# Kernel tuning notes

Hardware: AMD Instinct MI355X
Metric: run time of the kernel (lower is better)

Reference implementation:

```python
import jax, jax.numpy as jnp
import numpy as np

P = 3  # patchsize
EMB = 1024  # pretrain/target embed dimension


def adaptive_avg_pool1d(x, T):
    """torch.F.adaptive_avg_pool1d over last axis (static boundaries)."""
    L = x.shape[-1]
    i = np.arange(T)
    starts = (i * L) // T
    ends = -((-(i + 1) * L) // T)  # ceil((i+1)*L/T)
    cs = jnp.cumsum(x, axis=-1)
    cs = jnp.concatenate([jnp.zeros(x.shape[:-1] + (1,), x.dtype), cs], axis=-1)
    return (cs[..., ends] - cs[..., starts]) / jnp.asarray(ends - starts, x.dtype)


def patchify(x):
    """nn.Unfold(kernel=3, stride=1, pad=1): [B,C,H,W] -> [B,H*W,C,3,3]."""
    B, C, H, W = x.shape
    xp = jnp.pad(x, ((0, 0), (0, 0), (1, 1), (1, 1)))
    pats = jnp.stack([xp[:, :, i:i + H, j:j + W] for i in range(P) for j in range(P)], axis=2)
    pats = pats.reshape(B, C, P, P, H * W).transpose(0, 4, 1, 2, 3)
    return pats, (H, W)


def embed(feat2, feat3):
    B = feat2.shape[0]
    f2, (h0, w0) = patchify(feat2)   # [B, h0*w0, 512, 3, 3]
    f3, (h1, w1) = patchify(feat3)   # [B, h1*w1, 1024, 3, 3]
    C3 = feat3.shape[1]
    # align layer3 patch grid to layer2 grid (bilinear, align_corners=False)
    f3 = f3.reshape(B, h1, w1, C3, P, P).transpose(0, 3, 4, 5, 1, 2)
    f3 = f3.reshape(-1, h1, w1)
    f3 = jax.image.resize(f3, (f3.shape[0], h0, w0), method='bilinear')
    f3 = f3.reshape(B, C3, P, P, h0, w0).transpose(0, 4, 5, 1, 2, 3)
    f3 = f3.reshape(B, h0 * w0, C3, P, P)
    # Preprocessing: MeanMapper per layer -> [N, 2, 1024]
    feats = []
    for f in (f2, f3):
        flat = f.reshape(-1, 1, f.shape[-3] * P * P)       # [N, 1, C*9]
        feats.append(adaptive_avg_pool1d(flat, EMB)[:, 0, :])
    x = jnp.stack(feats, axis=1)                           # [N, 2, 1024]
    # Aggregator: adaptive pool over flattened [N, 1, 2048] -> [N, 1024]
    x = adaptive_avg_pool1d(x.reshape(x.shape[0], 1, -1), EMB)[:, 0, :]
    return x, (h0, w0)


def setup_inputs() -> dict:
    key = jax.random.key(0)
    k1, k2, k3 = jax.random.split(key, 3)
    feat2 = jax.random.normal(k1, (8, 512, 28, 28), dtype=jnp.float32)
    feat3 = jax.random.normal(k2, (8, 1024, 14, 14), dtype=jnp.float32)
    memory_bank = jax.random.normal(k3, (16384, 1024), dtype=jnp.float32)
    return {"feat2": feat2, "feat3": feat3, "memory_bank": memory_bank}


def reference(feat2, feat3, memory_bank):
    B = feat2.shape[0]
    q, (h0, w0) = embed(feat2, feat3)                      # [B*h0*w0, 1024]
    # squared-L2 1-NN against the memory bank (faiss IndexFlatL2, k=1)
    d2 = (jnp.sum(q * q, axis=-1, keepdims=True)
          - 2.0 * (q @ memory_bank.T)
          + jnp.sum(memory_bank * memory_bank, axis=-1)[None, :])
    patch_scores = jnp.min(d2, axis=-1).reshape(B, h0, w0)  # unpatch_scores
    image_scores = jnp.max(patch_scores.reshape(B, -1), axis=-1)  # PatchMaker.score
    return image_scores, patch_scores
```

## Files before the change

### kernel.cpp

```cpp
#include <hip/hip_runtime.h>
#include <hip/hip_bf16.h>

typedef signed char i8;
typedef unsigned char u8;
typedef unsigned short u16;
typedef unsigned int u32;
typedef __attribute__((ext_vector_type(4))) int i32x4;

#define GLD16(g, l) __builtin_amdgcn_global_load_lds((const __attribute__((address_space(1))) u32*)(g), (__attribute__((address_space(3))) u32*)(l), 16, 0, 0)

#define SB (4.5f / 127.f)
#define SQ (2.0f / 127.f)
#define INV_SB (127.f / 4.5f)
#define INV_SQ (127.f / 2.0f)
#define TWO_S (2.0f * SB * SQ)

__device__ __forceinline__ u32 flipf(float f) {
    u32 u = __float_as_uint(f);
    return (u >> 31) ? ~u : (u | 0x80000000u);
}

__device__ __forceinline__ float unflipf(u32 k) {
    return __uint_as_float((k >> 31) ? (k ^ 0x80000000u) : ~k);
}

__device__ __forceinline__ int q8(float x, float invs) {
    return __float2int_rn(fminf(fmaxf(x * invs, -127.f), 127.f));
}

__device__ __forceinline__ void taps(int o, int& i0, int& i1, float& w0, float& w1) {
    int k = (o - 1) >> 1;
    float fy = (0.5f * (float)o - 0.25f) - (float)k;
    i0 = k; i1 = k + 1;
    w0 = 1.0f - fy; w1 = fy;
    if (i0 < 0)  { i0 = 0;  w0 = 0.0f; w1 = 1.0f; }
    if (i1 > 13) { i1 = 13; w1 = 0.0f; w0 = 1.0f; }
}

__global__ __launch_bounds__(256) void prep_kernel(
    const float* __restrict__ f3, float* __restrict__ U,
    const float* __restrict__ mb, u8* __restrict__ mbb, float* __restrict__ mb2,
    u32* __restrict__ minkey, float* __restrict__ qn2) {
    int bid = blockIdx.x, tid = threadIdx.x;
    if (bid < 16384) {
        float4 v = ((const float4*)(mb + (size_t)bid * 1024))[tid];
        u32 p = ((u32)(u8)(i8)q8(v.x, INV_SB))
              | ((u32)(u8)(i8)q8(v.y, INV_SB) << 8)
              | ((u32)(u8)(i8)q8(v.z, INV_SB) << 16)
              | ((u32)(u8)(i8)q8(v.w, INV_SB) << 24);
        ((u32*)(mbb + (size_t)bid * 1024))[tid] = p;
        float ssq = v.x * v.x + v.y * v.y + v.z * v.z + v.w * v.w;
        for (int s = 32; s; s >>= 1) ssq += __shfl_down(ssq, s);
        __shared__ float sm[4];
        if ((tid & 63) == 0) sm[tid >> 6] = ssq;
        __syncthreads();
        if (tid == 0) mb2[bid] = sm[0] + sm[1] + sm[2] + sm[3];
        if (bid < 25) {
            int i = bid * 256 + tid;
            if (i < 6400) minkey[i] = 0xFFFFFFFFu;
        } else if (bid < 50) {
            int i = (bid - 25) * 256 + tid;
            if (i < 6272) qn2[i] = 0.f;
        }
    } else {
        int idx = (bid - 16384) * 256 + tid;
        if (idx >= 8 * 512 * 196) return;
        int b = idx / (512 * 196);
        int rem = idx % (512 * 196);
        int t = rem / 196;
        int yx = rem % 196;
        int y = yx / 14, x = yx % 14;
        const float* p0 = f3 + ((size_t)(b * 1024 + 2 * t)) * 196;
        const float* p1 = p0 + 196;
        float s = 0.f;
        #pragma unroll
        for (int dy = -1; dy <= 1; ++dy) {
            int yy = y + dy; if ((unsigned)yy >= 14u) continue;
            #pragma unroll
            for (int dx = -1; dx <= 1; ++dx) {
                int xx = x + dx; if ((unsigned)xx >= 14u) continue;
                s += p0[yy * 14 + xx] + p1[yy * 14 + xx];
            }
        }
        U[idx] = s;
    }
}

__global__ __launch_bounds__(256) void q_kernel(const float* __restrict__ feat2, const float* __restrict__ U,
                                                u8* __restrict__ qb, float* __restrict__ qn2) {
    __shared__ float lds[3 * 64 * 29];
    const int bid = blockIdx.x;
    const int tid = threadIdx.x;
    const int b = bid / (28 * 16);
    const int rem = bid % (28 * 16);
    const int h = rem / 16;
    const int chunk = rem % 16;
    const int lane = tid & 63;
    const int wg = tid >> 6;

    if (chunk < 8) {
        const int c0 = chunk * 64;
        for (int i = tid; i < 3 * 64 * 28; i += 256) {
            int r = i / 1792;
            int rr = i % 1792;
            int c = rr / 28, x = rr % 28;
            int y = h - 1 + r;
            lds[(r * 64 + c) * 29 + x] = ((unsigned)y < 28u)
                ? feat2[((size_t)(b * 512 + c0 + c) * 28 + y) * 28 + x] : 0.f;
        }
        __syncthreads();
        const float* rowp = &lds[lane * 29];
        #pragma unroll
        for (int wi = 0; wi < 7; ++wi) {
            const int w = wg * 7 + wi;
            float s = 0.f;
            #pragma unroll
            for (int r = 0; r < 3; ++r) {
                #pragma unroll
                for (int dx = -1; dx <= 1; ++dx) {
                    int x = w + dx;
                    if ((unsigned)x >= 28u) continue;
                    float wt = (r == 1 && dx == 0) ? 2.f : 1.f;
                    s += wt * rowp[r * 64 * 29 + x];
                }
            }
            float val = s * 0.1f;
            const int n = b * 784 + h * 28 + w;
            qb[(size_t)n * 1024 + c0 + lane] = (u8)(i8)q8(val, INV_SQ);
            float ss = val * val;
            for (int sft = 32; sft; sft >>= 1) ss += __shfl_down(ss, sft);
            if (lane == 0) atomicAdd(&qn2[n], ss);
        }
    } else {
        const int t0 = (chunk - 8) * 64;
        int y0, y1; float wy0, wy1;
        taps(h, y0, y1, wy0, wy1);
        for (int i = tid; i < 2 * 64 * 14; i += 256) {
            int r = i / 896;
            int rr = i % 896;
            int t = rr / 14, x = rr % 14;
            lds[(r * 64 + t) * 15 + x] =
                U[(size_t)(b * 512 + t0 + t) * 196 + (r ? y1 : y0) * 14 + x];
        }
        __syncthreads();
        const float* rp0 = &lds[lane * 15];
        const float* rp1 = &lds[(64 + lane) * 15];
        #pragma unroll
        for (int wi = 0; wi < 7; ++wi) {
            const int w = wg * 7 + wi;
            int x0, x1; float wx0, wx1;
            taps(w, x0, x1, wx0, wx1);
            float val = (wy0 * (wx0 * rp0[x0] + wx1 * rp0[x1])
                       + wy1 * (wx0 * rp1[x0] + wx1 * rp1[x1])) * (1.f / 18.f);
            const int n = b * 784 + h * 28 + w;
            qb[(size_t)n * 1024 + 512 + t0 + lane] = (u8)(i8)q8(val, INV_SQ);
            float ss = val * val;
            for (int sft = 32; sft; sft >>= 1) ss += __shfl_down(ss, sft);
            if (lane == 0) atomicAdd(&qn2[n], ss);
        }
    }
}

__global__ __launch_bounds__(512, 4) void gemm_min_kernel(
    const u8* __restrict__ qb, const u8* __restrict__ mbb,
    const float* __restrict__ qn2, const float* __restrict__ mb2,
    u32* __restrict__ minkeys) {
    __shared__ __align__(16) u8 As[2][8192];
    __shared__ __align__(16) u8 Bs[2][16384];
    __shared__ u32 rowmin[128];

    const int tid = threadIdx.x;
    const int wid = tid >> 6;
    const int lane = tid & 63;
    const int wm = wid >> 2;
    const int wn = wid & 3;

    const int flat = blockIdx.x;
    const int swz = (flat & 7) * 400 + (flat >> 3);
    const int q0 = (swz % 50) * 128;
    const int m0 = (swz / 50) * 256;

    const int rloc = wid * 16 + (lane >> 2);
    const int sslot = (lane & 3) ^ ((lane >> 3) & 3);
    const size_t gA  = (size_t)(q0 + rloc) * 1024 + sslot * 16;
    const size_t gB0 = (size_t)(m0 + rloc) * 1024 + sslot * 16;
    const size_t gB1 = (size_t)(m0 + 128 + rloc) * 1024 + sslot * 16;
    const u32 ldA = wid * 1024;
    const u32 ldB1 = 8192 + wid * 1024;

    #define STAGE(T) { const int _t = (T); \
        GLD16(qb + gA + _t * 64, &As[_t & 1][ldA]); \
        GLD16(mbb + gB0 + _t * 64, &Bs[_t & 1][ldA]); \
        GLD16(mbb + gB1 + _t * 64, &Bs[_t & 1][ldB1]); }

    const u32 arow = (u32)(wm * 64 + (lane & 15)) * 64;
    const u32 brow = (u32)(wn * 64 + (lane & 15)) * 64;
    const u32 sl = (u32)(((lane >> 4) ^ (((lane & 15) >> 1) & 3)) * 16);

    i32x4 acc[4][4] = {};
    i32x4 a[4], b[4];

    STAGE(0);
    asm volatile("s_waitcnt vmcnt(0)" ::: "memory");
    __builtin_amdgcn_s_barrier();
    __builtin_amdgcn_sched_barrier(0);

    for (int t = 0; t < 16; ++t) {
        const u8* Ab = &As[t & 1][0];
        const u8* Bb = &Bs[t & 1][0];

        #pragma unroll
        for (int m = 0; m < 4; ++m) a[m] = *(const i32x4*)&Ab[arow + m * 1024 + sl];
        #pragma unroll
        for (int n = 0; n < 4; ++n) b[n] = *(const i32x4*)&Bb[brow + n * 1024 + sl];

        if (t < 15) STAGE(t + 1)

        asm volatile("s_waitcnt lgkmcnt(2)" ::: "memory");
        __builtin_amdgcn_sched_barrier(0);
        __builtin_amdgcn_s_setprio(1);
        #pragma unroll
        for (int m = 0; m < 4; ++m)
            #pragma unroll
            for (int n = 0; n < 2; ++n)
                acc[m][n] = __builtin_amdgcn_mfma_i32_16x16x64_i8(a[m], b[n], acc[m][n], 0, 0, 0);
        __builtin_amdgcn_s_setprio(0);
        asm volatile("s_waitcnt lgkmcnt(0)" ::: "memory");
        __builtin_amdgcn_sched_barrier(0);
        __builtin_amdgcn_s_setprio(1);
        #pragma unroll
        for (int m = 0; m < 4; ++m)
            #pragma unroll
            for (int n = 2; n < 4; ++n)
                acc[m][n] = __builtin_amdgcn_mfma_i32_16x16x64_i8(a[m], b[n], acc[m][n], 0, 0, 0);
        __builtin_amdgcn_s_setprio(0);

        if (t < 15) { asm volatile("s_waitcnt vmcnt(0)" ::: "memory"); }
        __builtin_amdgcn_s_barrier();
        __builtin_amdgcn_sched_barrier(0);
    }

    if (tid < 128) rowmin[tid] = 0xFFFFFFFFu;
    __syncthreads();

    float mb2v[4];
    #pragma unroll
    for (int n = 0; n < 4; ++n) mb2v[n] = mb2[m0 + wn * 64 + n * 16 + (lane & 15)];

    #pragma unroll
    for (int m = 0; m < 4; ++m) {
        #pragma unroll
        for (int r = 0; r < 4; ++r) {
            const int qrow = wm * 64 + m * 16 + (lane >> 4) * 4 + r;
            const float qq = qn2[q0 + qrow];
            float v = 3.4e38f;
            #pragma unroll
            for (int n = 0; n < 4; ++n) {
                float d2 = qq + mb2v[n] - TWO_S * (float)acc[m][n][r];
                v = fminf(v, d2);
            }
            #pragma unroll
            for (int s = 1; s < 16; s <<= 1) v = fminf(v, __shfl_xor(v, s));
            if ((lane & 15) == 0) atomicMin(&rowmin[qrow], flipf(v));
        }
    }
    __syncthreads();
    if (tid < 128) atomicMin(minkeys + q0 + tid, rowmin[tid]);
}

__global__ __launch_bounds__(256) void final_kernel(const u32* __restrict__ keys, float* __restrict__ out) {
    int b = blockIdx.x, tid = threadIdx.x;
    float mx = -3.4e38f;
    for (int i = tid; i < 784; i += 256) {
        float f = unflipf(keys[b * 784 + i]);
        out[8 + b * 784 + i] = f;
        mx = fmaxf(mx, f);
    }
    for (int s = 32; s; s >>= 1) mx = fmaxf(mx, __shfl_down(mx, s));
    __shared__ float sm[4];
    if ((tid & 63) == 0) sm[tid >> 6] = mx;
    __syncthreads();
    if (tid == 0) out[b] = fmaxf(fmaxf(sm[0], sm[1]), fmaxf(sm[2], sm[3]));
}

extern "C" void kernel_launch(void* const* d_in, const int* in_sizes, int n_in,
                              void* d_out, int out_size, void* d_ws, size_t ws_size,
                              hipStream_t stream) {
    const float* feat2 = (const float*)d_in[0];
    const float* feat3 = (const float*)d_in[1];
    const float* mb    = (const float*)d_in[2];
    float* out = (float*)d_out;

    char* ws = (char*)d_ws;
    float* U      = (float*)(ws);
    u8*    qb     = (u8*)   (ws + 3211264);
    u8*    mbb    = (u8*)   (ws + 9764864);
    float* qn2    = (float*)(ws + 26542080);
    float* mb2    = (float*)(ws + 26567168);
    u32*   minkey = (u32*)  (ws + 26632704);

    prep_kernel<<<19520, 256, 0, stream>>>(feat3, U, mb, mbb, mb2, minkey, qn2);
    q_kernel<<<3584, 256, 0, stream>>>(feat2, U, qb, qn2);
    gemm_min_kernel<<<3200, 512, 0, stream>>>(qb, mbb, qn2, mb2, minkey);
    final_kernel<<<8, 256, 0, stream>>>(minkey, out);
}
```

Measured before the change: 186.2 us.

## Load GEMM A operand directly from global into registers, skipping LDS staging

```diff
diff --git a/kernel.cpp b/kernel.cpp
--- a/kernel.cpp
+++ b/kernel.cpp
@@ -165,7 +165,6 @@
     const u8* __restrict__ qb, const u8* __restrict__ mbb,
     const float* __restrict__ qn2, const float* __restrict__ mb2,
     u32* __restrict__ minkeys) {
-    __shared__ __align__(16) u8 As[2][8192];
     __shared__ __align__(16) u8 Bs[2][16384];
     __shared__ u32 rowmin[128];
 
@@ -182,63 +181,76 @@
 
     const int rloc = wid * 16 + (lane >> 2);
     const int sslot = (lane & 3) ^ ((lane >> 3) & 3);
-    const size_t gA  = (size_t)(q0 + rloc) * 1024 + sslot * 16;
     const size_t gB0 = (size_t)(m0 + rloc) * 1024 + sslot * 16;
     const size_t gB1 = (size_t)(m0 + 128 + rloc) * 1024 + sslot * 16;
-    const u32 ldA = wid * 1024;
+    const u32 ldB0 = wid * 1024;
     const u32 ldB1 = 8192 + wid * 1024;
 
-    #define STAGE(T) { const int _t = (T); \
-        GLD16(qb + gA + _t * 64, &As[_t & 1][ldA]); \
-        GLD16(mbb + gB0 + _t * 64, &Bs[_t & 1][ldA]); \
+    #define STAGE_B(T) { const int _t = (T); \
+        GLD16(mbb + gB0 + _t * 64, &Bs[_t & 1][ldB0]); \
         GLD16(mbb + gB1 + _t * 64, &Bs[_t & 1][ldB1]); }
 
-    const u32 arow = (u32)(wm * 64 + (lane & 15)) * 64;
     const u32 brow = (u32)(wn * 64 + (lane & 15)) * 64;
     const u32 sl = (u32)(((lane >> 4) ^ (((lane & 15) >> 1) & 3)) * 16);
 
+    const u8* aBase = qb + (size_t)(q0 + wm * 64) * 1024
+                    + (u32)(lane & 15) * 1024 + (u32)(lane >> 4) * 16;
+
+    #define LOAD_A(DST, T) { \
+        _Pragma("unroll") for (int m = 0; m < 4; ++m) \
+            DST[m] = *(const i32x4*)(aBase + m * 16384 + (T) * 64); }
+
     i32x4 acc[4][4] = {};
-    i32x4 a[4], b[4];
-
-    STAGE(0);
+    i32x4 aP[4], aQ[4], b[4];
+
+    #define MFMA_H(AC, N0) \
+        _Pragma("unroll") for (int m = 0; m < 4; ++m) \
+            _Pragma("unroll") for (int n = 0; n < 2; ++n) \
+                acc[m][(N0) + n] = __builtin_amdgcn_mfma_i32_16x16x64_i8(AC[m], b[(N0) + n], acc[m][(N0) + n], 0, 0, 0);
+
+    #define TILE_BODY(T, AC, AN, STG, PREF, LAST) { \
+        const u8* Bb = &Bs[(T) & 1][0]; \
+        _Pragma("unroll") for (int n = 0; n < 4; ++n) \
+            b[n] = *(const i32x4*)&Bb[brow + n * 1024 + sl]; \
+        if (STG) STAGE_B((T) + 1) \
+        if (PREF) LOAD_A(AN, (T) + 1) \
+        asm volatile("s_waitcnt lgkmcnt(2)" ::: "memory"); \
+        __builtin_amdgcn_sched_barrier(0); \
+        __builtin_amdgcn_s_setprio(1); \
+        MFMA_H(AC, 0); \
+        __builtin_amdgcn_s_setprio(0); \
+        asm volatile("s_waitcnt lgkmcnt(0)" ::: "memory"); \
+        __builtin_amdgcn_sched_barrier(0); \
+        __builtin_amdgcn_s_setprio(1); \
+        MFMA_H(AC, 2); \
+        __builtin_amdgcn_s_setprio(0); \
+        if (!LAST) { asm volatile("s_waitcnt vmcnt(0)" ::: "memory"); } \
+        __builtin_amdgcn_s_barrier(); \
+        __builtin_amdgcn_sched_barrier(0); \
+    }
+
+    STAGE_B(0)
+    LOAD_A(aP, 0)
     asm volatile("s_waitcnt vmcnt(0)" ::: "memory");
     __builtin_amdgcn_s_barrier();
     __builtin_amdgcn_sched_barrier(0);
 
-    for (int t = 0; t < 16; ++t) {
-        const u8* Ab = &As[t & 1][0];
-        const u8* Bb = &Bs[t & 1][0];
-
-        #pragma unroll
-        for (int m = 0; m < 4; ++m) a[m] = *(const i32x4*)&Ab[arow + m * 1024 + sl];
-        #pragma unroll
-        for (int n = 0; n < 4; ++n) b[n] = *(const i32x4*)&Bb[brow + n * 1024 + sl];
-
-        if (t < 15) STAGE(t + 1)
-
-        asm volatile("s_waitcnt lgkmcnt(2)" ::: "memory");
-        __builtin_amdgcn_sched_barrier(0);
-        __builtin_amdgcn_s_setprio(1);
-        #pragma unroll
-        for (int m = 0; m < 4; ++m)
-            #pragma unroll
-            for (int n = 0; n < 2; ++n)
-                acc[m][n] = __builtin_amdgcn_mfma_i32_16x16x64_i8(a[m], b[n], acc[m][n], 0, 0, 0);
-        __builtin_amdgcn_s_setprio(0);
-        asm volatile("s_waitcnt lgkmcnt(0)" ::: "memory");
-        __builtin_amdgcn_sched_barrier(0);
-        __builtin_amdgcn_s_setprio(1);
-        #pragma unroll
-        for (int m = 0; m < 4; ++m)
-            #pragma unroll
-            for (int n = 2; n < 4; ++n)
-                acc[m][n] = __builtin_amdgcn_mfma_i32_16x16x64_i8(a[m], b[n], acc[m][n], 0, 0, 0);
-        __builtin_amdgcn_s_setprio(0);
-
-        if (t < 15) { asm volatile("s_waitcnt vmcnt(0)" ::: "memory"); }
-        __builtin_amdgcn_s_barrier();
-        __builtin_amdgcn_sched_barrier(0);
-    }
+    TILE_BODY(0,  aP, aQ, 1, 1, 0)
+    TILE_BODY(1,  aQ, aP, 1, 1, 0)
+    TILE_BODY(2,  aP, aQ, 1, 1, 0)
+    TILE_BODY(3,  aQ, aP, 1, 1, 0)
+    TILE_BODY(4,  aP, aQ, 1, 1, 0)
+    TILE_BODY(5,  aQ, aP, 1, 1, 0)
+    TILE_BODY(6,  aP, aQ, 1, 1, 0)
+    TILE_BODY(7,  aQ, aP, 1, 1, 0)
+    TILE_BODY(8,  aP, aQ, 1, 1, 0)
+    TILE_BODY(9,  aQ, aP, 1, 1, 0)
+    TILE_BODY(10, aP, aQ, 1, 1, 0)
+    TILE_BODY(11, aQ, aP, 1, 1, 0)
+    TILE_BODY(12, aP, aQ, 1, 1, 0)
+    TILE_BODY(13, aQ, aP, 1, 1, 0)
+    TILE_BODY(14, aP, aQ, 1, 1, 0)
+    TILE_BODY(15, aQ, aP, 0, 0, 1)
 
     if (tid < 128) rowmin[tid] = 0xFFFFFFFFu;
     __syncthreads();
```

Result: slower. 310.8 us (+66.9%).

## Pre-tile int8 operands into MFMA fragment layout and load directly from global

Applied to the files above, without the earlier changes.

```diff
diff --git a/kernel.cpp b/kernel.cpp
--- a/kernel.cpp
+++ b/kernel.cpp
@@ -6,8 +6,6 @@
 typedef unsigned short u16;
 typedef unsigned int u32;
 typedef __attribute__((ext_vector_type(4))) int i32x4;
-
-#define GLD16(g, l) __builtin_amdgcn_global_load_lds((const __attribute__((address_space(1))) u32*)(g), (__attribute__((address_space(3))) u32*)(l), 16, 0, 0)
 
 #define SB (4.5f / 127.f)
 #define SQ (2.0f / 127.f)
@@ -37,9 +35,14 @@
     if (i1 > 13) { i1 = 13; w1 = 0.0f; w0 = 1.0f; }
 }
 
+__device__ __forceinline__ size_t qbt_addr(int n, int t, int lane) {
+    return (size_t)(n >> 4) * 16384 + (size_t)t * 1024
+         + (size_t)(n & 15) * 16 + (size_t)(lane >> 4) * 256 + (lane & 15);
+}
+
 __global__ __launch_bounds__(256) void prep_kernel(
     const float* __restrict__ f3, float* __restrict__ U,
-    const float* __restrict__ mb, u8* __restrict__ mbb, float* __restrict__ mb2,
+    const float* __restrict__ mb, u8* __restrict__ mbbT, float* __restrict__ mb2,
     u32* __restrict__ minkey, float* __restrict__ qn2) {
     int bid = blockIdx.x, tid = threadIdx.x;
     if (bid < 16384) {
@@ -48,7 +51,10 @@
               | ((u32)(u8)(i8)q8(v.y, INV_SB) << 8)
               | ((u32)(u8)(i8)q8(v.z, INV_SB) << 16)
               | ((u32)(u8)(i8)q8(v.w, INV_SB) << 24);
-        ((u32*)(mbb + (size_t)bid * 1024))[tid] = p;
+        size_t addr = (size_t)(bid >> 4) * 16384 + (size_t)(tid >> 4) * 1024
+                    + (size_t)(bid & 15) * 16 + (size_t)((tid >> 2) & 3) * 256
+                    + (size_t)((tid & 3) * 4);
+        *(u32*)(mbbT + addr) = p;
         float ssq = v.x * v.x + v.y * v.y + v.z * v.z + v.w * v.w;
         for (int s = 32; s; s >>= 1) ssq += __shfl_down(ssq, s);
         __shared__ float sm[4];
@@ -87,7 +93,7 @@
 }
 
 __global__ __launch_bounds__(256) void q_kernel(const float* __restrict__ feat2, const float* __restrict__ U,
-                                                u8* __restrict__ qb, float* __restrict__ qn2) {
+                                                u8* __restrict__ qbT, float* __restrict__ qn2) {
     __shared__ float lds[3 * 64 * 29];
     const int bid = blockIdx.x;
     const int tid = threadIdx.x;
@@ -126,7 +132,7 @@
             }
             float val = s * 0.1f;
             const int n = b * 784 + h * 28 + w;
-            qb[(size_t)n * 1024 + c0 + lane] = (u8)(i8)q8(val, INV_SQ);
+            qbT[qbt_addr(n, chunk, lane)] = (u8)(i8)q8(val, INV_SQ);
             float ss = val * val;
             for (int sft = 32; sft; sft >>= 1) ss += __shfl_down(ss, sft);
             if (lane == 0) atomicAdd(&qn2[n], ss);
@@ -153,7 +159,7 @@
             float val = (wy0 * (wx0 * rp0[x0] + wx1 * rp0[x1])
                        + wy1 * (wx0 * rp1[x0] + wx1 * rp1[x1])) * (1.f / 18.f);
             const int n = b * 784 + h * 28 + w;
-            qb[(size_t)n * 1024 + 512 + t0 + lane] = (u8)(i8)q8(val, INV_SQ);
+            qbT[qbt_addr(n, chunk, lane)] = (u8)(i8)q8(val, INV_SQ);
             float ss = val * val;
             for (int sft = 32; sft; sft >>= 1) ss += __shfl_down(ss, sft);
             if (lane == 0) atomicAdd(&qn2[n], ss);
@@ -162,11 +168,9 @@
 }
 
 __global__ __launch_bounds__(512, 4) void gemm_min_kernel(
-    const u8* __restrict__ qb, const u8* __restrict__ mbb,
+    const u8* __restrict__ qbT, const u8* __restrict__ mbbT,
     const float* __restrict__ qn2, const float* __restrict__ mb2,
     u32* __restrict__ minkeys) {
-    __shared__ __align__(16) u8 As[2][8192];
-    __shared__ __align__(16) u8 Bs[2][16384];
     __shared__ u32 rowmin[128];
 
     const int tid = threadIdx.x;
@@ -180,64 +184,24 @@
     const int q0 = (swz % 50) * 128;
     const int m0 = (swz / 50) * 256;
 
-    const int rloc = wid * 16 + (lane >> 2);
-    const int sslot = (lane & 3) ^ ((lane >> 3) & 3);
-    const size_t gA  = (size_t)(q0 + rloc) * 1024 + sslot * 16;
-    const size_t gB0 = (size_t)(m0 + rloc) * 1024 + sslot * 16;
-    const size_t gB1 = (size_t)(m0 + 128 + rloc) * 1024 + sslot * 16;
-    const u32 ldA = wid * 1024;
-    const u32 ldB1 = 8192 + wid * 1024;
-
-    #define STAGE(T) { const int _t = (T); \
-        GLD16(qb + gA + _t * 64, &As[_t & 1][ldA]); \
-        GLD16(mbb + gB0 + _t * 64, &Bs[_t & 1][ldA]); \
-        GLD16(mbb + gB1 + _t * 64, &Bs[_t & 1][ldB1]); }
-
-    const u32 arow = (u32)(wm * 64 + (lane & 15)) * 64;
-    const u32 brow = (u32)(wn * 64 + (lane & 15)) * 64;
-    const u32 sl = (u32)(((lane >> 4) ^ (((lane & 15) >> 1) & 3)) * 16);
+    const u8* aT = qbT  + ((size_t)(q0 >> 4) + wm * 4) * 16384 + (u32)lane * 16;
+    const u8* bT = mbbT + ((size_t)(m0 >> 4) + wn * 4) * 16384 + (u32)lane * 16;
 
     i32x4 acc[4][4] = {};
-    i32x4 a[4], b[4];
-
-    STAGE(0);
-    asm volatile("s_waitcnt vmcnt(0)" ::: "memory");
-    __builtin_amdgcn_s_barrier();
-    __builtin_amdgcn_sched_barrier(0);
 
     for (int t = 0; t < 16; ++t) {
-        const u8* Ab = &As[t & 1][0];
-        const u8* Bb = &Bs[t & 1][0];
-
-        #pragma unroll
-        for (int m = 0; m < 4; ++m) a[m] = *(const i32x4*)&Ab[arow + m * 1024 + sl];
-        #pragma unroll
-        for (int n = 0; n < 4; ++n) b[n] = *(const i32x4*)&Bb[brow + n * 1024 + sl];
-
-        if (t < 15) STAGE(t + 1)
-
-        asm volatile("s_waitcnt lgkmcnt(2)" ::: "memory");
-        __builtin_amdgcn_sched_barrier(0);
+        i32x4 a[4], b[4];
+        #pragma unroll
+        for (int m = 0; m < 4; ++m) a[m] = *(const i32x4*)(aT + m * 16384 + t * 1024);
+        #pragma unroll
+        for (int n = 0; n < 4; ++n) b[n] = *(const i32x4*)(bT + n * 16384 + t * 1024);
         __builtin_amdgcn_s_setprio(1);
         #pragma unroll
         for (int m = 0; m < 4; ++m)
             #pragma unroll
-            for (int n = 0; n < 2; ++n)
+            for (int n = 0; n < 4; ++n)
                 acc[m][n] = __builtin_amdgcn_mfma_i32_16x16x64_i8(a[m], b[n], acc[m][n], 0, 0, 0);
         __builtin_amdgcn_s_setprio(0);
-        asm volatile("s_waitcnt lgkmcnt(0)" ::: "memory");
-        __builtin_amdgcn_sched_barrier(0);
-        __builtin_amdgcn_s_setprio(1);
-        #pragma unroll
-        for (int m = 0; m < 4; ++m)
-            #pragma unroll
-            for (int n = 2; n < 4; ++n)
-                acc[m][n] = __builtin_amdgcn_mfma_i32_16x16x64_i8(a[m], b[n], acc[m][n], 0, 0, 0);
-        __builtin_amdgcn_s_setprio(0);
-
-        if (t < 15) { asm volatile("s_waitcnt vmcnt(0)" ::: "memory"); }
-        __builtin_amdgcn_s_barrier();
-        __builtin_amdgcn_sched_barrier(0);
     }
 
     if (tid < 128) rowmin[tid] = 0xFFFFFFFFu;
@@ -293,14 +257,14 @@
 
     char* ws = (char*)d_ws;
     float* U      = (float*)(ws);
-    u8*    qb     = (u8*)   (ws + 3211264);
-    u8*    mbb    = (u8*)   (ws + 9764864);
+    u8*    qbT    = (u8*)   (ws + 3211264);
+    u8*    mbbT   = (u8*)   (ws + 9764864);
     float* qn2    = (float*)(ws + 26542080);
     float* mb2    = (float*)(ws + 26567168);
     u32*   minkey = (u32*)  (ws + 26632704);
 
-    prep_kernel<<<19520, 256, 0, stream>>>(feat3, U, mb, mbb, mb2, minkey, qn2);
-    q_kernel<<<3584, 256, 0, stream>>>(feat2, U, qb, qn2);
-    gemm_min_kernel<<<3200, 512, 0, stream>>>(qb, mbb, qn2, mb2, minkey);
+    prep_kernel<<<19520, 256, 0, stream>>>(feat3, U, mb, mbbT, mb2, minkey, qn2);
+    q_kernel<<<3584, 256, 0, stream>>>(feat2, U, qbT, qn2);
+    gemm_min_kernel<<<3200, 512, 0, stream>>>(qbT, mbbT, qn2, mb2, minkey);
     final_kernel<<<8, 256, 0, stream>>>(minkey, out);
 }
```

Measured after the change: 214.2 us. 1.15x slower.
